# Performance work log

Hardware: AMD Instinct MI355X
Metric: run time of the kernel (lower is better)

Reference implementation:

```python
import jax, jax.numpy as jnp
import numpy as np

B, L, D, H = 2, 2048, 2048, 16
DH = D // H

def setup_inputs() -> dict:
    key = jax.random.key(0)
    ks = jax.random.split(key, 7)
    q = jax.random.normal(ks[0], (B, L, D), dtype=jnp.float32)
    k = jax.random.normal(ks[1], (B, L, D), dtype=jnp.float32)
    v = jax.random.normal(ks[2], (B, L, D), dtype=jnp.float32)
    # causal mask: True means masked (matches torch masked_fill semantics)
    attn_mask = jnp.triu(jnp.ones((L, L), dtype=bool), k=1)[None, None, :, :]
    scale = 0.02
    wq = jax.random.normal(ks[3], (D, D), dtype=jnp.float32) * scale
    wk = jax.random.normal(ks[4], (D, D), dtype=jnp.float32) * scale
    wv = jax.random.normal(ks[5], (D, D), dtype=jnp.float32) * scale
    wo = jax.random.normal(ks[6], (D, D), dtype=jnp.float32) * scale
    return {"q": q, "k": k, "v": v, "attn_mask": attn_mask,
            "wq": wq, "wk": wk, "wv": wv, "wo": wo}

def _split_heads(x):
    b, l, _ = x.shape
    return x.reshape(b, l, H, DH).transpose(0, 2, 1, 3)  # [B,H,L,DH]

def reference(q, k, v, attn_mask, wq, wk, wv, wo):
    # torch Linear: y = x @ W.T (bias=False)
    qh = _split_heads(q @ wq.T)
    kh = _split_heads(k @ wk.T)
    vh = _split_heads(v @ wv.T)
    scale = 1.0 / np.sqrt(DH).astype(np.float32)
    scores = jnp.einsum('bhqd,bhkd->bhqk', qh, kh) * scale
    neg = jnp.finfo(scores.dtype).min
    scores = jnp.where(attn_mask, neg, scores)
    attn = jax.nn.softmax(scores, axis=-1)
    ctx = jnp.einsum('bhqk,bhkd->bhqd', attn, vh)
    ctx = ctx.transpose(0, 2, 1, 3).reshape(q.shape[0], q.shape[1], D)
    return ctx @ wo.T
```

## Files before the change

kernel.cpp:

```cpp
#include <hip/hip_runtime.h>

#define B_  2
#define L_  2048
#define D_  2048
#define H_  16
#define DH_ 128
#define K_  2048

typedef __attribute__((ext_vector_type(8))) short bf16x8;
typedef __attribute__((ext_vector_type(4))) float f32x4;
typedef __attribute__((ext_vector_type(4))) float float4v;
typedef __attribute__((ext_vector_type(8))) unsigned short u16x8;
typedef __attribute__((ext_vector_type(4))) unsigned short u16x4;

__device__ __forceinline__ unsigned short f2bf(float f) {
  unsigned u = __builtin_bit_cast(unsigned, f);
  u += 0x7fffu + ((u >> 16) & 1u);
  return (unsigned short)(u >> 16);
}

typedef __attribute__((address_space(3))) unsigned int lds_uint;
typedef __attribute__((address_space(1))) const unsigned int glob_uint;
__device__ __forceinline__ void gld16(const void* g, void* l) {
  __builtin_amdgcn_global_load_lds((glob_uint*)g, (lds_uint*)l, 16, 0, 0);
}

#define BAR() do { asm volatile("" ::: "memory"); __builtin_amdgcn_s_barrier(); asm volatile("" ::: "memory"); } while (0)
#define VMCNT(n) asm volatile("s_waitcnt vmcnt(" #n ")" ::: "memory")

__global__ void cvt_all(const float* __restrict__ wq, const float* __restrict__ wk,
                        const float* __restrict__ wv, const float* __restrict__ wo,
                        const float* __restrict__ q, const float* __restrict__ k,
                        const float* __restrict__ v, unsigned short* __restrict__ ws,
                        int nacts) {
  const size_t DD = (size_t)D_ * D_;
  const size_t BLD = (size_t)B_ * L_ * D_;
  const int z = blockIdx.z;
  const float* src;
  unsigned short* dst;
  size_t nelem;
  if (z < 4) {
    src = (z == 0) ? wq : (z == 1) ? wk : (z == 2) ? wv : wo;
    dst = ws + (size_t)z * DD;
    nelem = DD;
  } else {
    if (z - 4 >= nacts) return;
    src = (z == 4) ? q : (z == 5) ? k : v;
    dst = ws + 4 * DD + (size_t)(z - 4) * BLD;
    nelem = BLD;
  }
  size_t i = ((size_t)blockIdx.x * 256 + threadIdx.x) * 8;
  if (i >= nelem) return;
  float4v x0 = *(const float4v*)(src + i);
  float4v x1 = *(const float4v*)(src + i + 4);
  u16x8 p;
  p[0]=f2bf(x0[0]); p[1]=f2bf(x0[1]); p[2]=f2bf(x0[2]); p[3]=f2bf(x0[3]);
  p[4]=f2bf(x1[0]); p[5]=f2bf(x1[1]); p[6]=f2bf(x1[2]); p[7]=f2bf(x1[3]);
  *(u16x8*)(dst + i) = p;
}

template <int KIND>
__global__ __launch_bounds__(512, 2) void gemm8(
    const unsigned short* __restrict__ a0, const unsigned short* __restrict__ a1,
    const unsigned short* __restrict__ a2,
    const unsigned short* __restrict__ w0, const unsigned short* __restrict__ w1,
    const unsigned short* __restrict__ w2,
    unsigned short* __restrict__ Qh, unsigned short* __restrict__ Kh,
    unsigned short* __restrict__ Vt, float* __restrict__ OF) {
  __shared__ unsigned short smem[3 * 24576];

  const int lin = blockIdx.x + 32 * (blockIdx.y + 8 * blockIdx.z);
  const int cpx = KIND ? 32 : 96;
  const int s = (lin & 7) * cpx + (lin >> 3);
  const int mt = s & 31;
  const int r_ = s >> 5;
  const int ntile = KIND ? r_ : (r_ & 7);
  const int z = KIND ? 0 : (r_ >> 3);

  const unsigned short* A = KIND ? a0 : (z == 0 ? a0 : z == 1 ? a1 : a2);
  const unsigned short* W = KIND ? w0 : (z == 0 ? w0 : z == 1 ? w1 : w2);
  const int mode = KIND ? 2 : (z == 2 ? 1 : 0);

  const int bm0 = mt * 128;
  const int bn0 = ntile * 256;

  const int tid = threadIdx.x;
  const int wid = tid >> 6, lane = tid & 63;
  const int wr = wid >> 2, wc = wid & 3;
  const int l15 = lane & 15, l4 = lane >> 4;

  const unsigned short* gsrc[6];
  int ldst[6];
  {
#pragma unroll
    for (int i = 0; i < 2; ++i) {
      const int c = i * 512 + tid, r = c >> 3, s0 = c & 7;
      gsrc[i] = A + (size_t)(bm0 + r) * K_ + ((s0 ^ (r & 7)) << 3);
      ldst[i] = c * 8;
    }
#pragma unroll
    for (int u = 0; u < 2; ++u)
#pragma unroll
      for (int i = 0; i < 2; ++i) {
        const int c = i * 512 + tid, r = c >> 3, s0 = c & 7;
        gsrc[2 + u * 2 + i] = W + (size_t)(bn0 + u * 128 + r) * K_ + ((s0 ^ (r & 7)) << 3);
        ldst[2 + u * 2 + i] = 8192 + (u * 1024 + c) * 8;
      }
  }
#define STAGE(idx, p) do { gld16(gsrc[idx], &smem[(p) * 24576 + ldst[idx]]); gsrc[idx] += 64; } while (0)

  int offA[2][2][2], offB[4][2];
#pragma unroll
  for (int mh = 0; mh < 2; ++mh)
#pragma unroll
    for (int ml = 0; ml < 2; ++ml)
#pragma unroll
      for (int ks = 0; ks < 2; ++ks) {
        const int row = wr * 64 + mh * 32 + ml * 16 + l15;
        const int ch = ks * 4 + l4;
        offA[mh][ml][ks] = row * 64 + ((ch ^ (row & 7)) << 3);
      }
#pragma unroll
  for (int nf = 0; nf < 4; ++nf)
#pragma unroll
    for (int ks = 0; ks < 2; ++ks) {
      const int rowb = wc * 64 + nf * 16 + l15;
      const int ch = ks * 4 + l4;
      offB[nf][ks] = 8192 + rowb * 64 + ((ch ^ (rowb & 7)) << 3);
    }

  f32x4 acc[4][4];
#pragma unroll
  for (int m = 0; m < 4; ++m)
#pragma unroll
    for (int n = 0; n < 4; ++n) { f32x4 zz = {0.f, 0.f, 0.f, 0.f}; acc[m][n] = zz; }

  STAGE(0, 0); STAGE(1, 0); STAGE(2, 0); STAGE(3, 0); STAGE(4, 0); STAGE(5, 0);
  STAGE(0, 1); STAGE(1, 1); STAGE(2, 1); STAGE(3, 1); STAGE(4, 1); STAGE(5, 1);
  VMCNT(6);
  BAR();

  int p = 0;
  for (int t = 0; t < 32; ++t) {
    int p2 = p + 2; if (p2 >= 3) p2 -= 3;
    const unsigned short* bA = &smem[p * 24576];
    bf16x8 af[2][2], bfr[4][2];
#pragma unroll
    for (int ml = 0; ml < 2; ++ml)
#pragma unroll
      for (int ks = 0; ks < 2; ++ks)
        af[ml][ks] = *(const bf16x8*)&bA[offA[0][ml][ks]];
#pragma unroll
    for (int nf = 0; nf < 4; ++nf)
#pragma unroll
      for (int ks = 0; ks < 2; ++ks)
        bfr[nf][ks] = *(const bf16x8*)&bA[offB[nf][ks]];
    if (t < 30) { STAGE(0, p2); STAGE(1, p2); STAGE(2, p2); STAGE(3, p2); }
    BAR();
    __builtin_amdgcn_s_setprio(1);
#pragma unroll
    for (int ml = 0; ml < 2; ++ml)
#pragma unroll
      for (int nf = 0; nf < 4; ++nf)
#pragma unroll
        for (int ks = 0; ks < 2; ++ks)
          acc[ml][nf] = __builtin_amdgcn_mfma_f32_16x16x32_bf16(af[ml][ks], bfr[nf][ks], acc[ml][nf], 0, 0, 0);
    __builtin_amdgcn_s_setprio(0);
    BAR();
#pragma unroll
    for (int ml = 0; ml < 2; ++ml)
#pragma unroll
      for (int ks = 0; ks < 2; ++ks)
        af[ml][ks] = *(const bf16x8*)&bA[offA[1][ml][ks]];
    if (t < 30) { STAGE(4, p2); STAGE(5, p2); }
    BAR();
    __builtin_amdgcn_s_setprio(1);
#pragma unroll
    for (int ml = 0; ml < 2; ++ml)
#pragma unroll
      for (int nf = 0; nf < 4; ++nf)
#pragma unroll
        for (int ks = 0; ks < 2; ++ks)
          acc[2 + ml][nf] = __builtin_amdgcn_mfma_f32_16x16x32_bf16(af[ml][ks], bfr[nf][ks], acc[2 + ml][nf], 0, 0, 0);
    __builtin_amdgcn_s_setprio(0);
    if (t < 30) { VMCNT(6); } else { VMCNT(0); }
    BAR();
    p = (p == 2) ? 0 : p + 1;
  }
#undef STAGE

  if (mode == 0) {
    unsigned short* O = (z == 0) ? Qh : Kh;
#pragma unroll
    for (int mf = 0; mf < 4; ++mf) {
      const int rr = bm0 + wr * 64 + mf * 16 + l4 * 4;
#pragma unroll
      for (int nf = 0; nf < 4; ++nf) {
        const int cc = bn0 + wc * 64 + nf * 16 + l15;
        const int h = cc >> 7, dh = cc & 127;
#pragma unroll
        for (int j = 0; j < 4; ++j) {
          const int r2 = rr + j;
          O[((size_t)((r2 >> 11) * H_ + h) * L_ + (r2 & 2047)) * DH_ + dh] = f2bf(acc[mf][nf][j]);
        }
      }
    }
  } else if (mode == 1) {
    unsigned short* T = smem;
#pragma unroll
    for (int mf = 0; mf < 4; ++mf) {
      const int rl = wr * 64 + mf * 16 + l4 * 4;
#pragma unroll
      for (int nf = 0; nf < 4; ++nf) {
        const int cl = wc * 64 + nf * 16 + l15;
        u16x4 vv;
#pragma unroll
        for (int j = 0; j < 4; ++j) vv[j] = f2bf(acc[mf][nf][j]);
        *(u16x4*)&T[cl * 128 + (((rl >> 3) ^ (cl & 7)) << 3) + (rl & 7)] = vv;
      }
    }
    __syncthreads();
    const int b = bm0 >> 11, lbase = bm0 & 2047;
#pragma unroll
    for (int it = 0; it < 8; ++it) {
      const int idx = it * 512 + tid;
      const int rT = idx >> 4, sT = idx & 15;
      u16x8 val = *(const u16x8*)&T[rT * 128 + ((sT ^ (rT & 7)) << 3)];
      const int n = bn0 + rT, h = n >> 7, dh = n & 127;
      *(u16x8*)&Vt[((size_t)(b * H_ + h) * DH_ + dh) * L_ + lbase + sT * 8] = val;
    }
  } else {
#pragma unroll
    for (int mf = 0; mf < 4; ++mf) {
      const int rr = bm0 + wr * 64 + mf * 16 + l4 * 4;
#pragma unroll
      for (int nf = 0; nf < 4; ++nf) {
        const int cc = bn0 + wc * 64 + nf * 16 + l15;
#pragma unroll
        for (int j = 0; j < 4; ++j) OF[(size_t)(rr + j) * D_ + cc] = acc[mf][nf][j];
      }
    }
  }
}

__global__ __launch_bounds__(256, 2) void proj_gemm_f32a(
    const float* __restrict__ q, const float* __restrict__ k, const float* __restrict__ v,
    const unsigned short* __restrict__ wqb, const unsigned short* __restrict__ wkb,
    const unsigned short* __restrict__ wvb,
    unsigned short* __restrict__ Qh, unsigned short* __restrict__ Kh,
    unsigned short* __restrict__ Vt) {
  __shared__ unsigned short smem[128 * 136];
  unsigned short* As = smem;
  unsigned short* Bs = smem + 128 * 64;

  const int z = blockIdx.z;
  const float* A = (z == 0) ? q : (z == 1) ? k : v;
  const unsigned short* W = (z == 0) ? wqb : (z == 1) ? wkb : wvb;

  const int tid = threadIdx.x;
  const int wave = tid >> 6, lane = tid & 63;
  const int wr = wave >> 1, wc = wave & 1;
  const int bm0 = blockIdx.x * 128;
  const int bn0 = blockIdx.y * 128;
  const int l15 = lane & 15, l4 = lane >> 4;

  f32x4 acc[4][4];
#pragma unroll
  for (int m = 0; m < 4; m++)
#pragma unroll
    for (int n = 0; n < 4; n++) { f32x4 zz = {0.f, 0.f, 0.f, 0.f}; acc[m][n] = zz; }

  for (int k0 = 0; k0 < K_; k0 += 64) {
#pragma unroll
    for (int it = 0; it < 4; ++it) {
      const int base = it * 256 + wave * 64;
      const int ch = base + lane;
      const int r = ch >> 3, c = ch & 7;
      gld16(W + (size_t)(bn0 + r) * K_ + (k0 + c * 8), Bs + base * 8);
    }
#pragma unroll
    for (int it = 0; it < 4; ++it) {
      const int ch = it * 256 + tid;
      const int r = ch >> 3, c = ch & 7;
      const float* g = A + (size_t)(bm0 + r) * K_ + (k0 + c * 8);
      float4v x0 = *(const float4v*)g;
      float4v x1 = *(const float4v*)(g + 4);
      u16x8 pp;
      pp[0]=f2bf(x0[0]); pp[1]=f2bf(x0[1]); pp[2]=f2bf(x0[2]); pp[3]=f2bf(x0[3]);
      pp[4]=f2bf(x1[0]); pp[5]=f2bf(x1[1]); pp[6]=f2bf(x1[2]); pp[7]=f2bf(x1[3]);
      *(u16x8*)&As[ch * 8] = pp;
    }
    __syncthreads();
#pragma unroll
    for (int ks = 0; ks < 2; ++ks) {
      const int kc = ks * 32 + l4 * 8;
      bf16x8 af[4], bfr[4];
#pragma unroll
      for (int m = 0; m < 4; m++) af[m] = *(const bf16x8*)&As[(wr * 64 + m * 16 + l15) * 64 + kc];
#pragma unroll
      for (int n = 0; n < 4; n++) bfr[n] = *(const bf16x8*)&Bs[(wc * 64 + n * 16 + l15) * 64 + kc];
#pragma unroll
      for (int m = 0; m < 4; m++)
#pragma unroll
        for (int n = 0; n < 4; n++)
          acc[m][n] = __builtin_amdgcn_mfma_f32_16x16x32_bf16(af[m], bfr[n], acc[m][n], 0, 0, 0);
    }
    __syncthreads();
  }

  if (z < 2) {
    unsigned short* O = (z == 0) ? Qh : Kh;
#pragma unroll
    for (int m = 0; m < 4; m++) {
      const int rr = bm0 + wr * 64 + m * 16 + l4 * 4;
#pragma unroll
      for (int n = 0; n < 4; n++) {
        const int cc = bn0 + wc * 64 + n * 16 + l15;
        const int h = cc >> 7, dh = cc & 127;
#pragma unroll
        for (int j = 0; j < 4; j++) {
          const int r2 = rr + j;
          O[((size_t)((r2 >> 11) * H_ + h) * L_ + (r2 & 2047)) * DH_ + dh] = f2bf(acc[m][n][j]);
        }
      }
    }
  } else {
    __syncthreads();
    unsigned short* T = smem;
#pragma unroll
    for (int m = 0; m < 4; m++)
#pragma unroll
      for (int n = 0; n < 4; n++) {
        const int cl = wc * 64 + n * 16 + l15;
        const int rl = wr * 64 + m * 16 + l4 * 4;
#pragma unroll
        for (int j = 0; j < 4; j++) T[cl * 136 + rl + j] = f2bf(acc[m][n][j]);
      }
    __syncthreads();
    const int b = bm0 >> 11, lbase = bm0 & 2047;
    const int hb = bn0 >> 7;
#pragma unroll
    for (int it = 0; it < 8; ++it) {
      const int idx = it * 256 + tid;
      const int dhl = idx >> 4, c = idx & 15;
      u16x8 val = *(const u16x8*)&T[dhl * 136 + c * 8];
      *(u16x8*)&Vt[((size_t)(b * H_ + hb) * DH_ + dhl) * L_ + lbase + c * 8] = val;
    }
  }
}

#define SCALE_ 0.08838834764831845f

__global__ __launch_bounds__(256, 2) void attn_kernel(
    const unsigned short* __restrict__ Qh, const unsigned short* __restrict__ Kh,
    const unsigned short* __restrict__ Vt, unsigned short* __restrict__ ctx) {
  __shared__ unsigned short Ks[128 * 128];
  __shared__ unsigned short Vs[128 * 128];
  __shared__ unsigned short Ps[4][16 * 128];

  const int pair = blockIdx.x, bh = blockIdx.y;
  const size_t hoff = (size_t)bh * L_ * DH_;
  const unsigned short* Qp = Qh + hoff;
  const unsigned short* Kp = Kh + hoff;
  const unsigned short* Vp = Vt + hoff;

  const int tid = threadIdx.x, wave = tid >> 6, lane = tid & 63;
  const int l15 = lane & 15, l4 = lane >> 4;
  const int b = bh >> 4, h = bh & 15;

#pragma unroll 1
  for (int p = 0; p < 2; ++p) {
    const int qt = p ? (31 - pair) : pair;
    const int ntiles = (qt + 2) >> 1;

    bf16x8 qf[4];
    {
      const int qrow = qt * 64 + wave * 16 + l15;
#pragma unroll
      for (int s = 0; s < 4; s++)
        qf[s] = *(const bf16x8*)&Qp[(size_t)qrow * DH_ + s * 32 + l4 * 8];
    }

    f32x4 o[8];
#pragma unroll
    for (int df = 0; df < 8; df++) { f32x4 zz = {0.f, 0.f, 0.f, 0.f}; o[df] = zz; }
    float m_r[4] = {-1e30f, -1e30f, -1e30f, -1e30f};
    float l_r[4] = {0.f, 0.f, 0.f, 0.f};

    for (int kt = 0; kt < ntiles; ++kt) {
#pragma unroll
      for (int it = 0; it < 8; ++it) {
        const int base = it * 256 + wave * 64;
        const int ch = base + lane;
        const int r = ch >> 4, s = ch & 15;
        gld16(Kp + (size_t)(kt * 128 + r) * DH_ + ((s ^ (r & 7)) * 8), (unsigned short*)Ks + base * 8);
      }
#pragma unroll
      for (int it = 0; it < 8; ++it) {
        const int base = it * 256 + wave * 64;
        const int ch = base + lane;
        const int r = ch >> 4, s = ch & 15;
        gld16(Vp + (size_t)r * L_ + kt * 128 + ((s ^ (r & 7)) * 8), (unsigned short*)Vs + base * 8);
      }
      __syncthreads();

      f32x4 sa[8];
#pragma unroll
      for (int f = 0; f < 8; f++) { f32x4 zz = {0.f, 0.f, 0.f, 0.f}; sa[f] = zz; }
      __builtin_amdgcn_s_setprio(1);
#pragma unroll
      for (int ks = 0; ks < 4; ++ks) {
        const int c = ks * 4 + l4;
#pragma unroll
        for (int f = 0; f < 8; ++f) {
          const int n = f * 16 + l15;
          bf16x8 kf = *(const bf16x8*)&Ks[n * 128 + ((c ^ (n & 7)) * 8)];
          sa[f] = __builtin_amdgcn_mfma_f32_16x16x32_bf16(qf[ks], kf, sa[f], 0, 0, 0);
        }
      }
      __builtin_amdgcn_s_setprio(0);

      const bool last = (kt == ntiles - 1);
#pragma unroll
      for (int f = 0; f < 8; f++) {
        const int kg = kt * 128 + f * 16 + l15;
#pragma unroll
        for (int j = 0; j < 4; j++) {
          float t = sa[f][j] * SCALE_;
          if (last && kg > qt * 64 + wave * 16 + l4 * 4 + j) t = -1e30f;
          sa[f][j] = t;
        }
      }

#pragma unroll
      for (int j = 0; j < 4; j++) {
        float mx = fmaxf(fmaxf(fmaxf(sa[0][j], sa[1][j]), fmaxf(sa[2][j], sa[3][j])),
                         fmaxf(fmaxf(sa[4][j], sa[5][j]), fmaxf(sa[6][j], sa[7][j])));
#pragma unroll
        for (int d = 1; d < 16; d <<= 1) mx = fmaxf(mx, __shfl_xor(mx, d));
        const float mnew = fmaxf(m_r[j], mx);
        const float alpha = __expf(m_r[j] - mnew);
        float rs = 0.f;
        const int row = l4 * 4 + j;
#pragma unroll
        for (int f = 0; f < 8; f++) {
          float pp = __expf(sa[f][j] - mnew);
          rs += pp;
          const int col = f * 16 + l15;
          const int c = col >> 3;
          Ps[wave][row * 128 + ((c ^ (row & 7)) * 8) + (col & 7)] = f2bf(pp);
        }
#pragma unroll
        for (int d = 1; d < 16; d <<= 1) rs += __shfl_xor(rs, d);
        l_r[j] = l_r[j] * alpha + rs;
        m_r[j] = mnew;
#pragma unroll
        for (int df = 0; df < 8; df++) o[df][j] *= alpha;
      }

      __builtin_amdgcn_s_setprio(1);
#pragma unroll
      for (int ksl = 0; ksl < 4; ++ksl) {
        const int pc = ksl * 4 + l4;
        bf16x8 pf = *(const bf16x8*)&Ps[wave][l15 * 128 + ((pc ^ (l15 & 7)) * 8)];
#pragma unroll
        for (int df = 0; df < 8; ++df) {
          const int vr = df * 16 + l15;
          bf16x8 vf = *(const bf16x8*)&Vs[vr * 128 + ((pc ^ (vr & 7)) * 8)];
          o[df] = __builtin_amdgcn_mfma_f32_16x16x32_bf16(pf, vf, o[df], 0, 0, 0);
        }
      }
      __builtin_amdgcn_s_setprio(0);
      __syncthreads();
    }

#pragma unroll
    for (int j = 0; j < 4; j++) {
      const float inv = 1.0f / l_r[j];
      const int lq = qt * 64 + wave * 16 + l4 * 4 + j;
      const size_t rowb = ((size_t)(b * L_ + lq)) * D_ + h * DH_;
#pragma unroll
      for (int df = 0; df < 8; ++df)
        ctx[rowb + df * 16 + l15] = f2bf(o[df][j] * inv);
    }
  }
}

extern "C" void kernel_launch(void* const* d_in, const int* in_sizes, int n_in,
                              void* d_out, int out_size, void* d_ws, size_t ws_size,
                              hipStream_t stream) {
  const float* q  = (const float*)d_in[0];
  const float* k  = (const float*)d_in[1];
  const float* v  = (const float*)d_in[2];
  const float* wq = (const float*)d_in[4];
  const float* wk = (const float*)d_in[5];
  const float* wv = (const float*)d_in[6];
  const float* wo = (const float*)d_in[7];

  const size_t DD = (size_t)D_ * D_;
  const size_t BLD = (size_t)B_ * L_ * D_;
  unsigned short* ws  = (unsigned short*)d_ws;
  unsigned short* wqb = ws;
  unsigned short* wkb = wqb + DD;
  unsigned short* wvb = wkb + DD;
  unsigned short* wob = wvb + DD;

  const size_t need_full = (4 * DD + 7 * BLD) * 2;

  if (ws_size >= need_full) {
    unsigned short* qb  = wob + DD;
    unsigned short* kb  = qb + BLD;
    unsigned short* vb  = kb + BLD;
    unsigned short* QhP = vb + BLD;
    unsigned short* KhP = QhP + BLD;
    unsigned short* VtP = KhP + BLD;
    unsigned short* ctx = VtP + BLD;

    cvt_all<<<dim3(4096, 1, 7), 256, 0, stream>>>(wq, wk, wv, wo, q, k, v, ws, 3);
    gemm8<0><<<dim3(32, 8, 3), 512, 0, stream>>>(qb, kb, vb, wqb, wkb, wvb, QhP, KhP, VtP, nullptr);
    attn_kernel<<<dim3(16, 32), 256, 0, stream>>>(QhP, KhP, VtP, ctx);
    gemm8<1><<<dim3(32, 8, 1), 512, 0, stream>>>(ctx, nullptr, nullptr, wob, nullptr, nullptr,
                                                 nullptr, nullptr, nullptr, (float*)d_out);
  } else {
    unsigned short* QhP = wob + DD;
    unsigned short* KhP = QhP + BLD;
    unsigned short* VtP = KhP + BLD;
    unsigned short* ctx = VtP + BLD;

    cvt_all<<<dim3(4096, 1, 4), 256, 0, stream>>>(wq, wk, wv, wo, q, k, v, ws, 0);
    proj_gemm_f32a<<<dim3(32, 16, 3), 256, 0, stream>>>(q, k, v, wqb, wkb, wvb, QhP, KhP, VtP);
    attn_kernel<<<dim3(16, 32), 256, 0, stream>>>(QhP, KhP, VtP, ctx);
    gemm8<1><<<dim3(32, 8, 1), 512, 0, stream>>>(ctx, nullptr, nullptr, wob, nullptr, nullptr,
                                                 nullptr, nullptr, nullptr, (float*)d_out);
  }
}
```

Before: 291.3 us.

## Enlarge attention query tile to 128 rows with 512 threads; merge GEMM k-halves

The attention kernel now runs 8 waves per block, so each block covers 128 query rows instead of 64. Each K/V tile loaded into LDS is therefore reused by twice as many queries, and the grid shrinks to 8x32 blocks. The GEMM main loop loads all A fragments up front and issues all 32 MFMAs in one phase, dropping two barriers per iteration at the cost of more live registers. The V transpose scratch switches from an XOR swizzle to a padded stride of 136. Risks are lower occupancy and fewer blocks for load balancing in the causal attention.

```diff
diff --git a/kernel.cpp b/kernel.cpp
--- a/kernel.cpp
+++ b/kernel.cpp
@@ -109,17 +109,15 @@
   }
 #define STAGE(idx, p) do { gld16(gsrc[idx], &smem[(p) * 24576 + ldst[idx]]); gsrc[idx] += 64; } while (0)
 
-  int offA[2][2][2], offB[4][2];
-#pragma unroll
-  for (int mh = 0; mh < 2; ++mh)
-#pragma unroll
-    for (int ml = 0; ml < 2; ++ml)
-#pragma unroll
-      for (int ks = 0; ks < 2; ++ks) {
-        const int row = wr * 64 + mh * 32 + ml * 16 + l15;
-        const int ch = ks * 4 + l4;
-        offA[mh][ml][ks] = row * 64 + ((ch ^ (row & 7)) << 3);
-      }
+  int offA[4][2], offB[4][2];
+#pragma unroll
+  for (int mf = 0; mf < 4; ++mf)
+#pragma unroll
+    for (int ks = 0; ks < 2; ++ks) {
+      const int row = wr * 64 + mf * 16 + l15;
+      const int ch = ks * 4 + l4;
+      offA[mf][ks] = row * 64 + ((ch ^ (row & 7)) << 3);
+    }
 #pragma unroll
   for (int nf = 0; nf < 4; ++nf)
 #pragma unroll
@@ -144,44 +142,26 @@
   for (int t = 0; t < 32; ++t) {
     int p2 = p + 2; if (p2 >= 3) p2 -= 3;
     const unsigned short* bA = &smem[p * 24576];
-    bf16x8 af[2][2], bfr[4][2];
-#pragma unroll
-    for (int ml = 0; ml < 2; ++ml)
+    bf16x8 af[4][2], bfr[4][2];
+#pragma unroll
+    for (int mf = 0; mf < 4; ++mf)
 #pragma unroll
       for (int ks = 0; ks < 2; ++ks)
-        af[ml][ks] = *(const bf16x8*)&bA[offA[0][ml][ks]];
+        af[mf][ks] = *(const bf16x8*)&bA[offA[mf][ks]];
 #pragma unroll
     for (int nf = 0; nf < 4; ++nf)
 #pragma unroll
       for (int ks = 0; ks < 2; ++ks)
         bfr[nf][ks] = *(const bf16x8*)&bA[offB[nf][ks]];
-    if (t < 30) { STAGE(0, p2); STAGE(1, p2); STAGE(2, p2); STAGE(3, p2); }
-    BAR();
+    if (t < 30) { STAGE(0, p2); STAGE(1, p2); STAGE(2, p2); STAGE(3, p2); STAGE(4, p2); STAGE(5, p2); }
     __builtin_amdgcn_s_setprio(1);
 #pragma unroll
-    for (int ml = 0; ml < 2; ++ml)
+    for (int mf = 0; mf < 4; ++mf)
 #pragma unroll
       for (int nf = 0; nf < 4; ++nf)
 #pragma unroll
         for (int ks = 0; ks < 2; ++ks)
-          acc[ml][nf] = __builtin_amdgcn_mfma_f32_16x16x32_bf16(af[ml][ks], bfr[nf][ks], acc[ml][nf], 0, 0, 0);
-    __builtin_amdgcn_s_setprio(0);
-    BAR();
-#pragma unroll
-    for (int ml = 0; ml < 2; ++ml)
-#pragma unroll
-      for (int ks = 0; ks < 2; ++ks)
-        af[ml][ks] = *(const bf16x8*)&bA[offA[1][ml][ks]];
-    if (t < 30) { STAGE(4, p2); STAGE(5, p2); }
-    BAR();
-    __builtin_amdgcn_s_setprio(1);
-#pragma unroll
-    for (int ml = 0; ml < 2; ++ml)
-#pragma unroll
-      for (int nf = 0; nf < 4; ++nf)
-#pragma unroll
-        for (int ks = 0; ks < 2; ++ks)
-          acc[2 + ml][nf] = __builtin_amdgcn_mfma_f32_16x16x32_bf16(af[ml][ks], bfr[nf][ks], acc[2 + ml][nf], 0, 0, 0);
+          acc[mf][nf] = __builtin_amdgcn_mfma_f32_16x16x32_bf16(af[mf][ks], bfr[nf][ks], acc[mf][nf], 0, 0, 0);
     __builtin_amdgcn_s_setprio(0);
     if (t < 30) { VMCNT(6); } else { VMCNT(0); }
     BAR();
@@ -216,7 +196,7 @@
         u16x4 vv;
 #pragma unroll
         for (int j = 0; j < 4; ++j) vv[j] = f2bf(acc[mf][nf][j]);
-        *(u16x4*)&T[cl * 128 + (((rl >> 3) ^ (cl & 7)) << 3) + (rl & 7)] = vv;
+        *(u16x4*)&T[cl * 136 + rl] = vv;
       }
     }
     __syncthreads();
@@ -224,10 +204,10 @@
 #pragma unroll
     for (int it = 0; it < 8; ++it) {
       const int idx = it * 512 + tid;
-      const int rT = idx >> 4, sT = idx & 15;
-      u16x8 val = *(const u16x8*)&T[rT * 128 + ((sT ^ (rT & 7)) << 3)];
+      const int rT = idx >> 4, cT = idx & 15;
+      u16x8 val = *(const u16x8*)&T[rT * 136 + cT * 8];
       const int n = bn0 + rT, h = n >> 7, dh = n & 127;
-      *(u16x8*)&Vt[((size_t)(b * H_ + h) * DH_ + dh) * L_ + lbase + sT * 8] = val;
+      *(u16x8*)&Vt[((size_t)(b * H_ + h) * DH_ + dh) * L_ + lbase + cT * 8] = val;
     }
   } else {
 #pragma unroll
@@ -351,12 +331,12 @@
 
 #define SCALE_ 0.08838834764831845f
 
-__global__ __launch_bounds__(256, 2) void attn_kernel(
+__global__ __launch_bounds__(512, 2) void attn_kernel(
     const unsigned short* __restrict__ Qh, const unsigned short* __restrict__ Kh,
     const unsigned short* __restrict__ Vt, unsigned short* __restrict__ ctx) {
   __shared__ unsigned short Ks[128 * 128];
   __shared__ unsigned short Vs[128 * 128];
-  __shared__ unsigned short Ps[4][16 * 128];
+  __shared__ unsigned short Ps[8][16 * 128];
 
   const int pair = blockIdx.x, bh = blockIdx.y;
   const size_t hoff = (size_t)bh * L_ * DH_;
@@ -370,12 +350,12 @@
 
 #pragma unroll 1
   for (int p = 0; p < 2; ++p) {
-    const int qt = p ? (31 - pair) : pair;
-    const int ntiles = (qt + 2) >> 1;
+    const int qt = p ? (15 - pair) : pair;
+    const int ntiles = qt + 1;
 
     bf16x8 qf[4];
     {
-      const int qrow = qt * 64 + wave * 16 + l15;
+      const int qrow = qt * 128 + wave * 16 + l15;
 #pragma unroll
       for (int s = 0; s < 4; s++)
         qf[s] = *(const bf16x8*)&Qp[(size_t)qrow * DH_ + s * 32 + l4 * 8];
@@ -389,18 +369,16 @@
 
     for (int kt = 0; kt < ntiles; ++kt) {
 #pragma unroll
-      for (int it = 0; it < 8; ++it) {
-        const int base = it * 256 + wave * 64;
-        const int ch = base + lane;
+      for (int it = 0; it < 4; ++it) {
+        const int ch = it * 512 + tid;
         const int r = ch >> 4, s = ch & 15;
-        gld16(Kp + (size_t)(kt * 128 + r) * DH_ + ((s ^ (r & 7)) * 8), (unsigned short*)Ks + base * 8);
-      }
-#pragma unroll
-      for (int it = 0; it < 8; ++it) {
-        const int base = it * 256 + wave * 64;
-        const int ch = base + lane;
+        gld16(Kp + (size_t)(kt * 128 + r) * DH_ + ((s ^ (r & 7)) * 8), (unsigned short*)Ks + ch * 8);
+      }
+#pragma unroll
+      for (int it = 0; it < 4; ++it) {
+        const int ch = it * 512 + tid;
         const int r = ch >> 4, s = ch & 15;
-        gld16(Vp + (size_t)r * L_ + kt * 128 + ((s ^ (r & 7)) * 8), (unsigned short*)Vs + base * 8);
+        gld16(Vp + (size_t)r * L_ + kt * 128 + ((s ^ (r & 7)) * 8), (unsigned short*)Vs + ch * 8);
       }
       __syncthreads();
 
@@ -420,14 +398,14 @@
       }
       __builtin_amdgcn_s_setprio(0);
 
-      const bool last = (kt == ntiles - 1);
+      const bool last = (kt == qt);
 #pragma unroll
       for (int f = 0; f < 8; f++) {
         const int kg = kt * 128 + f * 16 + l15;
 #pragma unroll
         for (int j = 0; j < 4; j++) {
           float t = sa[f][j] * SCALE_;
-          if (last && kg > qt * 64 + wave * 16 + l4 * 4 + j) t = -1e30f;
+          if (last && kg > qt * 128 + wave * 16 + l4 * 4 + j) t = -1e30f;
           sa[f][j] = t;
         }
       }
@@ -477,7 +455,7 @@
 #pragma unroll
     for (int j = 0; j < 4; j++) {
       const float inv = 1.0f / l_r[j];
-      const int lq = qt * 64 + wave * 16 + l4 * 4 + j;
+      const int lq = qt * 128 + wave * 16 + l4 * 4 + j;
       const size_t rowb = ((size_t)(b * L_ + lq)) * D_ + h * DH_;
 #pragma unroll
       for (int df = 0; df < 8; ++df)
@@ -518,7 +496,7 @@
 
     cvt_all<<<dim3(4096, 1, 7), 256, 0, stream>>>(wq, wk, wv, wo, q, k, v, ws, 3);
     gemm8<0><<<dim3(32, 8, 3), 512, 0, stream>>>(qb, kb, vb, wqb, wkb, wvb, QhP, KhP, VtP, nullptr);
-    attn_kernel<<<dim3(16, 32), 256, 0, stream>>>(QhP, KhP, VtP, ctx);
+    attn_kernel<<<dim3(8, 32), 512, 0, stream>>>(QhP, KhP, VtP, ctx);
     gemm8<1><<<dim3(32, 8, 1), 512, 0, stream>>>(ctx, nullptr, nullptr, wob, nullptr, nullptr,
                                                  nullptr, nullptr, nullptr, (float*)d_out);
   } else {
@@ -529,7 +507,7 @@
 
     cvt_all<<<dim3(4096, 1, 4), 256, 0, stream>>>(wq, wk, wv, wo, q, k, v, ws, 0);
     proj_gemm_f32a<<<dim3(32, 16, 3), 256, 0, stream>>>(q, k, v, wqb, wkb, wvb, QhP, KhP, VtP);
-    attn_kernel<<<dim3(16, 32), 256, 0, stream>>>(QhP, KhP, VtP, ctx);
+    attn_kernel<<<dim3(8, 32), 512, 0, stream>>>(QhP, KhP, VtP, ctx);
     gemm8<1><<<dim3(32, 8, 1), 512, 0, stream>>>(ctx, nullptr, nullptr, wob, nullptr, nullptr,
                                                  nullptr, nullptr, nullptr, (float*)d_out);
   }
```

New measurement: 286.5 us. No clear change (-1.6%).
